# Optimization experiments

Hardware: AMD Instinct MI355X
Metric: run time of the kernel (lower is better)

The kernel has to match this reference:

```python
import jax, jax.numpy as jnp
from jax import lax
import numpy as np

B, C, H, W = 4, 128, 256, 256
HEADS = 8
MID = 256


def conv2d(x, w, stride=1, pad=0, groups=1, mode='zeros'):
    if pad:
        m = 'reflect' if mode == 'reflect' else 'constant'
        x = jnp.pad(x, ((0, 0), (0, 0), (pad, pad), (pad, pad)), mode=m)
    return lax.conv_general_dilated(
        x, w, (stride, stride), 'VALID',
        dimension_numbers=('NCHW', 'OIHW', 'NCHW'),
        feature_group_count=groups)


def layernorm(x, w, b, eps=1e-5):
    # torch LayerNorm over channel dim (applied to b (hw) c layout)
    mu = jnp.mean(x, axis=1, keepdims=True)
    var = jnp.mean((x - mu) ** 2, axis=1, keepdims=True)
    xn = (x - mu) * lax.rsqrt(var + eps)
    return xn * w[None, :, None, None] + b[None, :, None, None]


def l2norm(x, eps=1e-12):
    n = jnp.sqrt(jnp.sum(x * x, axis=-1, keepdims=True))
    return x / jnp.maximum(n, eps)


def setup_inputs() -> dict:
    key = jax.random.key(0)
    ks = jax.random.split(key, 20)
    s = 0.02
    inp = {
        'x': jax.random.normal(ks[0], (B, C, H, W), jnp.float32),
        'illu_feat': jax.random.uniform(ks[1], (B, C, H, W), jnp.float32),
        'ln1_w': jnp.ones((C,), jnp.float32),
        'ln1_b': jnp.zeros((C,), jnp.float32),
        'q_w': jax.random.normal(ks[2], (C, 1, 3, 3), jnp.float32) * s,
        'k_w': jax.random.normal(ks[3], (C, C, 3, 3), jnp.float32) * s,
        'v_w': jax.random.normal(ks[4], (C, C, 1, 1), jnp.float32) * s,
        'a1_w': jax.random.normal(ks[5], (C, 1, 3, 3), jnp.float32) * s,
        'a2_w': jax.random.normal(ks[6], (C // 2, C, 1, 1), jnp.float32) * s,
        'a2_b': jnp.zeros((C // 2,), jnp.float32),
        'temp_a': jnp.ones((HEADS, 1, 1), jnp.float32),
        'temp_v': jnp.ones((HEADS, 1, 1), jnp.float32),
        'po_w': jax.random.normal(ks[7], (C, C, 1, 1), jnp.float32) * s,
        'ln2_w': jnp.ones((C,), jnp.float32),
        'ln2_b': jnp.zeros((C,), jnp.float32),
        'p1_w': jax.random.normal(ks[8], (MID, C, 1, 1), jnp.float32) * s,
        'p1_b': jnp.zeros((MID,), jnp.float32),
        'dw_w': jax.random.normal(ks[9], (MID, 1, 3, 3), jnp.float32) * s,
        'dw_b': jnp.zeros((MID,), jnp.float32),
        'p2_w': jax.random.normal(ks[10], (C, MID, 1, 1), jnp.float32) * s,
        'p2_b': jnp.zeros((C,), jnp.float32),
    }
    return inp


def reference(x, illu_feat, ln1_w, ln1_b, q_w, k_w, v_w, a1_w, a2_w, a2_b,
              temp_a, temp_v, po_w, ln2_w, ln2_b, p1_w, p1_b, dw_w, dw_b,
              p2_w, p2_b):
    b, c, h, w = x.shape
    # ---- Attention branch ----
    xn = layernorm(x, ln1_w, ln1_b)
    q = conv2d(xn, q_w, stride=2, pad=1, groups=c, mode='reflect')  # (b,c,h/2,w/2)
    k = conv2d(xn, k_w, stride=2, pad=1, mode='reflect')            # (b,c,h/2,w/2)
    v = conv2d(xn, v_w) * illu_feat                                 # (b,c,h,w)
    a = conv2d(conv2d(xn, a1_w, stride=2, pad=1, groups=c, mode='reflect'), a2_w)
    a = a + a2_b[None, :, None, None]                               # (b,c/2,h/2,w/2)

    h2, w2 = q.shape[-2:]
    l4 = h2 * w2
    cp = c // HEADS            # channels per head (q,k,v)
    ca = (c // 2) // HEADS     # channels per head (a)
    qr = l2norm(q.reshape(b, HEADS, cp, l4))
    kr = l2norm(k.reshape(b, HEADS, cp, l4))
    ar = l2norm(a.reshape(b, HEADS, ca, l4))
    vr = v.reshape(b, HEADS, cp, h * w)

    attn_a = jax.nn.softmax(jnp.einsum('bhcl,bhdl->bhcd', qr, ar) * temp_a, axis=-1)
    attn_k = jax.nn.softmax(jnp.einsum('bhdl,bhcl->bhdc', ar, kr) * temp_v, axis=-1)
    out_v = jnp.einsum('bhdc,bhcm->bhdm', attn_k, vr)   # (b,h,ca,HW)
    out = jnp.einsum('bhcd,bhdm->bhcm', attn_a, out_v)  # (b,h,cp,HW)
    out = out.reshape(b, c, h, w)
    x = x + conv2d(out, po_w)

    # ---- FFN branch ----
    y = layernorm(x, ln2_w, ln2_b)
    y = conv2d(y, p1_w) + p1_b[None, :, None, None]
    y = conv2d(y, dw_w, pad=1, groups=MID) + dw_b[None, :, None, None]
    y = jax.nn.relu(y)
    y = conv2d(y, p2_w) + p2_b[None, :, None, None]
    return x + y
```

## Files before the change

kernel.cpp:

```cpp
#include <hip/hip_runtime.h>

#define BB 4
#define CC 128
#define HH 256
#define WW 256
#define HWSZ 65536
#define H2 128
#define W2 128
#define L4SZ 16384
#define MIDC 256
#define NHEADS 8

typedef __attribute__((ext_vector_type(8))) short short8;
typedef __attribute__((ext_vector_type(4))) short s16x4;
typedef __attribute__((ext_vector_type(4))) float f32x4;
typedef __attribute__((ext_vector_type(4))) unsigned u32x4;
typedef __attribute__((ext_vector_type(2))) unsigned u32x2;

__device__ __forceinline__ short f2bf(float v) {
  unsigned u = __builtin_bit_cast(unsigned, v);
  u += 0x7fffu + ((u >> 16) & 1u);
  return (short)(u >> 16);
}
__device__ __forceinline__ unsigned pk2(float a, float b) {
// ... 197 lines not shown
      int slot = g ^ ((p >> 1) & 3);
      short8 bfrag = ldsb[p * 4 + slot];
      const short* wbase = wt + (tap * 128 + (lane & 15)) * 128 + ci0 + g * 8;
#pragma unroll
      for (int m = 0; m < 8; m++) {
        short8 afrag = *(const short8*)(wbase + m * 16 * 128);
        acc[m] = __builtin_amdgcn_mfma_f32_16x16x32_bf16(afrag, bfrag, acc[m], 0, 0, 0);
      }
    }
  }
  int oy = by * 8 + py, ox = bx * 8 + pxx;
  int rb = g * 4;
#pragma unroll
  for (int m = 0; m < 8; m++)
#pragma unroll
    for (int r = 0; r < 4; r++)
      kg[(size_t)(bi * CC + m * 16 + rb + r) * L4SZ + oy * W2 + ox] = f2bf(acc[m][r]);
}

__global__ __launch_bounds__(256) void k_a2(const short* __restrict__ a1g,
                                            const float* __restrict__ w,
                                            const float* __restrict__ bias,
                                            short* __restrict__ ab) {
  __shared__ float t[CC][64];
  int blk = blockIdx.x;
  int bi = blk >> 8;
  int p0 = (blk & 255) * 64;
  for (int i = threadIdx.x; i < CC * 64; i += 256) {
    int ci = i >> 6, px = i & 63;
    t[ci][px] = b2f(a1g[(size_t)(bi * CC + ci) * L4SZ + p0 + px]);
  }
  __syncthreads();
  int px = threadIdx.x & 63;
  int co0 = ((__builtin_amdgcn_readfirstlane((int)threadIdx.x)) >> 6) << 4;
  float acc[16];
#pragma unroll
  for (int j = 0; j < 16; j++) acc[j] = 0.f;
  for (int ci = 0; ci < CC; ci++) {
    float in = t[ci][px];
#pragma unroll
    for (int j = 0; j < 16; j++) acc[j] += w[(co0 + j) * CC + ci] * in;
  }
#pragma unroll
  for (int j = 0; j < 16; j++)
    ab[(size_t)(bi * 64 + co0 + j) * L4SZ + p0 + px] = f2bf(acc[j] + bias[co0 + j]);
}

__global__ __launch_bounds__(256) void k_gram(const short* __restrict__ qg,
                                              const short* __restrict__ kg,
                                              const short* __restrict__ ag,
                                              float* __restrict__ partial) {
  __shared__ float red[4][1280];
  int blk = blockIdx.x;
  int bh = blk >> 3, chunk = blk & 7;
  int b = bh >> 3, h = bh & 7;
  int tid = threadIdx.x, lane = tid & 63, wv = tid >> 6;
  int cl = lane & 15, g = lane >> 4;
  const short* qb = qg + (size_t)(b * 128 + h * 16 + cl) * L4SZ;
  const short* kb = kg + (size_t)(b * 128 + h * 16 + cl) * L4SZ;
  const short* ar = ag + (size_t)(b * 64 + h * 8 + cl) * L4SZ;
  int k0 = chunk * 2048 + wv * 512 + g * 8;
  f32x4 t0 = {0,0,0,0}, t1 = {0,0,0,0}, t2 = {0,0,0,0}, t3 = {0,0,0,0}, t4 = {0,0,0,0};
#pragma unroll 4
  for (int ks = 0; ks < 16; ks++) {
    int ko = k0 + ks * 32;
    short8 fq = *(const short8*)(qb + ko);
    short8 fk = *(const short8*)(kb + ko);
    short8 fa = *(const short8*)(ar + ko);
    t0 = __builtin_amdgcn_mfma_f32_16x16x32_bf16(fq, fa, t0, 0, 0, 0);
    t1 = __builtin_amdgcn_mfma_f32_16x16x32_bf16(fa, fk, t1, 0, 0, 0);
    t2 = __builtin_amdgcn_mfma_f32_16x16x32_bf16(fq, fq, t2, 0, 0, 0);
    t3 = __builtin_amdgcn_mfma_f32_16x16x32_bf16(fk, fk, t3, 0, 0, 0);
    t4 = __builtin_amdgcn_mfma_f32_16x16x32_bf16(fa, fa, t4, 0, 0, 0);
  }
#pragma unroll
  for (int r = 0; r < 4; r++) {
    int flat = (g * 4 + r) * 16 + cl;
    red[wv][flat]        = t0[r];
    red[wv][256 + flat]  = t1[r];
    red[wv][512 + flat]  = t2[r];
    red[wv][768 + flat]  = t3[r];
    red[wv][1024 + flat] = t4[r];
  }
  __syncthreads();
  float* po = partial + (size_t)(bh * 8 + chunk) * 1280;
  for (int i = tid; i < 1280; i += 256)
    po[i] = red[0][i] + red[1][i] + red[2][i] + red[3][i];
}

__global__ __launch_bounds__(64) void k_softmax2(const float* __restrict__ partial,
                                                 const float* __restrict__ tA,
                                                 const float* __restrict__ tV,
                                                 float* __restrict__ attnA,
                                                 float* __restrict__ attnK) {
  __shared__ float S[1280];
  int bh = blockIdx.x;
  int h = bh & 7;
  for (int i = threadIdx.x; i < 1280; i += 64) {
    float s = 0.f;
    for (int c = 0; c < 8; c++) s += partial[(size_t)(bh * 8 + c) * 1280 + i];
    S[i] = s;
  }
  __syncthreads();
  float ta = tA[h], tv = tV[h];
  if (threadIdx.x < 16) {
    int c = threadIdx.x;
    float nq = fmaxf(sqrtf(S[512 + c * 17]), 1e-12f);
    float lg[8]; float m = -1e30f;
#pragma unroll
    for (int e = 0; e < 8; e++) {
      float na = fmaxf(sqrtf(S[1024 + e * 17]), 1e-12f);
      lg[e] = S[c * 16 + e] / (nq * na) * ta;
      m = fmaxf(m, lg[e]);
    }
    float sum = 0.f;
#pragma unroll
    for (int e = 0; e < 8; e++) { lg[e] = expf(lg[e] - m); sum += lg[e]; }
    float inv = 1.f / sum;
#pragma unroll
    for (int e = 0; e < 8; e++) attnA[(bh * 16 + c) * 8 + e] = lg[e] * inv;
  } else if (threadIdx.x < 24) {
    int e = threadIdx.x - 16;
    float na = fmaxf(sqrtf(S[1024 + e * 17]), 1e-12f);
    float lg[16]; float m = -1e30f;
#pragma unroll
    for (int c = 0; c < 16; c++) {
      float nk = fmaxf(sqrtf(S[768 + c * 17]), 1e-12f);
      lg[c] = S[256 + e * 16 + c] / (na * nk) * tv;
      m = fmaxf(m, lg[c]);
    }
    float sum = 0.f;
#pragma unroll
    for (int c = 0; c < 16; c++) { lg[c] = expf(lg[c] - m); sum += lg[c]; }
    float inv = 1.f / sum;
#pragma unroll
    for (int c = 0; c < 16; c++) attnK[(bh * 8 + e) * 16 + c] = lg[c] * inv;
  }
}

__global__ __launch_bounds__(256) void k_vx2(const short* __restrict__ xnt,
                                             const float* __restrict__ illu,
                                             const float* __restrict__ x,
                                             const short* __restrict__ vwb,
                                             const short* __restrict__ Mb,
                                             u32x4* __restrict__ x2n4,
                                             float* __restrict__ mu,
                                             float* __restrict__ rs) {
  __shared__ unsigned lds[4608];
  int blk = blockIdx.x;
  int bi = blk >> 10, p0 = (blk & 1023) * 64;
  int tid = threadIdx.x, lane = tid & 63, wv = tid >> 6;
  int cl = lane & 15, g = lane >> 4;
  int px = wv * 16 + cl;
  const u32x4* xsrc = (const u32x4*)(xnt + ((size_t)(bi * HWSZ + p0) << 7));
  for (int it = 0; it < 4; it++) {
    int idx = it * 256 + tid;
    int pp = idx >> 4, gg = idx & 15;
    u32x4 v = xsrc[pp * 16 + gg];
    ((u32x4*)lds)[pp * 16 + (gg ^ (pp & 7))] = v;
  }
  __syncthreads();
  f32x4 acc[8];
#pragma unroll
  for (int m = 0; m < 8; m++) acc[m] = (f32x4){0.f, 0.f, 0.f, 0.f};
#pragma unroll
  for (int kc = 0; kc < 4; kc++) {
    short8 bf = *(const short8*)((const short*)lds + px * 128 + (((kc * 4 + g) ^ (px & 7)) * 8));
#pragma unroll
    for (int m = 0; m < 8; m++) {
      short8 af = *(const short8*)(vwb + (m * 16 + cl) * 128 + kc * 32 + g * 8);
      acc[m] = __builtin_amdgcn_mfma_f32_16x16x32_bf16(af, bf, acc[m], 0, 0, 0);
    }
  }
  __syncthreads();
#pragma unroll
  for (int m = 0; m < 8; m++) {
    int cob = m * 16 + g * 4;
    float v0 = acc[m][0] * illu[(size_t)(bi * CC + cob + 0) * HWSZ + p0 + px];
    float v1 = acc[m][1] * illu[(size_t)(bi * CC + cob + 1) * HWSZ + p0 + px];
    float v2 = acc[m][2] * illu[(size_t)(bi * CC + cob + 2) * HWSZ + p0 + px];
    float v3 = acc[m][3] * illu[(size_t)(bi * CC + cob + 3) * HWSZ + p0 + px];
    int gi = 2 * m + (g >> 1);
    unsigned* dst = lds + px * 64 + ((gi ^ (px & 7)) << 2) + (g & 1) * 2;
    dst[0] = pk2(v0, v1);
    dst[1] = pk2(v2, v3);
  }
  __syncthreads();
  f32x4 acc2[8];
#pragma unroll
  for (int m = 0; m < 8; m++) acc2[m] = (f32x4){0.f, 0.f, 0.f, 0.f};
  const short* Mbb = Mb + bi * 16384;
#pragma unroll
  for (int kc = 0; kc < 4; kc++) {
    short8 bf = *(const short8*)((const short*)lds + px * 128 + (((kc * 4 + g) ^ (px & 7)) * 8));
#pragma unroll
    for (int m = 0; m < 8; m++) {
      short8 af = *(const short8*)(Mbb + (m * 16 + cl) * 128 + kc * 32 + g * 8);
      acc2[m] = __builtin_amdgcn_mfma_f32_16x16x32_bf16(af, bf, acc2[m], 0, 0, 0);
    }
  }
  float s = 0.f, s2 = 0.f;
  unsigned xp[16];
#pragma unroll
  for (int m = 0; m < 8; m++) {
    float tv[4];
#pragma unroll
    for (int r = 0; r < 4; r++) {
      int co = m * 16 + g * 4 + r;
      size_t gi = (size_t)(bi * CC + co) * HWSZ + p0 + px;
      float t = x[gi] + acc2[m][r];
      tv[r] = t; s += t; s2 += t * t;
    }
    xp[2 * m]     = pk2(tv[0], tv[1]);
    xp[2 * m + 1] = pk2(tv[2], tv[3]);
  }
  s  += __shfl_xor(s, 16);  s  += __shfl_xor(s, 32);
  s2 += __shfl_xor(s2, 16); s2 += __shfl_xor(s2, 32);
  float muv = s * (1.f / 128.f);
  float rsv = rsqrtf(s2 * (1.f / 128.f) - muv * muv + 1e-5f);
  if (g == 0) { mu[bi * HWSZ + p0 + px] = muv; rs[bi * HWSZ + p0 + px] = rsv; }
  __syncthreads();
#pragma unroll
  for (int m = 0; m < 8; m++) {
    lds[px * 68 + m * 8 + g * 2 + 0] = xp[2 * m];
    lds[px * 68 + m * 8 + g * 2 + 1] = xp[2 * m + 1];
  }
  __syncthreads();
  u32x4* dst4 = x2n4 + (size_t)(bi * HWSZ + p0) * 16;
  for (int it = 0; it < 4; it++) {
    int flat = it * 256 + tid;
    int pp = flat >> 4, j = flat & 15;
    dst4[flat] = *(const u32x4*)(lds + pp * 68 + j * 4);
  }
}

__global__ __launch_bounds__(256) void k_p1(const u32x4* __restrict__ x2n4,
                                            const short* __restrict__ w1p,
                                            const float* __restrict__ s1,
                                            const float* __restrict__ s2f,
                                            const float* __restrict__ mu,
                                            const float* __restrict__ rs,
                                            u32x4* __restrict__ y1n4) {
  __shared__ u32x4 bt[1024];
  __shared__ u32x4 olds[2048];
  int blk = blockIdx.x;
  int bi = blk >> 10, p0 = (blk & 1023) * 64;
  int tid = threadIdx.x, lane = tid & 63, wv = tid >> 6;
  int cl = lane & 15, g = lane >> 4;
  for (int f = tid; f < 1024; f += 256) {
    int px = f >> 4, kg = f & 15;
    bt[kg * 64 + (px ^ kg)] = x2n4[(size_t)(bi * HWSZ + p0 + px) * 16 + kg];
  }
  __syncthreads();
  f32x4 acc[4][4];
#pragma unroll
  for (int mt = 0; mt < 4; mt++)
#pragma unroll
    for (int n = 0; n < 4; n++) acc[mt][n] = (f32x4){0.f, 0.f, 0.f, 0.f};
#pragma unroll
  for (int kc = 0; kc < 4; kc++) {
    short8 bfr[4];
#pragma unroll
    for (int n = 0; n < 4; n++) {
      int px = n * 16 + cl, kgi = kc * 4 + g;
      bfr[n] = __builtin_bit_cast(short8, bt[kgi * 64 + (px ^ kgi)]);
    }
#pragma unroll
    for (int mt = 0; mt < 4; mt++) {
      short8 af = *(const short8*)(w1p + (wv * 64 + mt * 16 + cl) * 128 + kc * 32 + g * 8);
#pragma unroll
      for (int n = 0; n < 4; n++)
        acc[mt][n] = __builtin_amdgcn_mfma_f32_16x16x32_bf16(af, bfr[n], acc[mt][n], 0, 0, 0);
    }
  }
  float muv[4], rsv[4];
#pragma unroll
  for (int n = 0; n < 4; n++) {
    muv[n] = mu[bi * HWSZ + p0 + n * 16 + cl];
    rsv[n] = rs[bi * HWSZ + p0 + n * 16 + cl];
  }
#pragma unroll
  for (int mt = 0; mt < 4; mt++) {
    int mid = wv * 64 + mt * 16 + g * 4;
    float4 s1v = *(const float4*)(s1 + mid);
    float4 s2v = *(const float4*)(s2f + mid);
    int gi = wv * 8 + mt * 2 + (g >> 1);
#pragma unroll
    for (int n = 0; n < 4; n++) {
      int px = n * 16 + cl;
      float y0 = rsv[n] * (acc[mt][n][0] - muv[n] * s1v.x) + s2v.x;
      float y1 = rsv[n] * (acc[mt][n][1] - muv[n] * s1v.y) + s2v.y;
      float y2 = rsv[n] * (acc[mt][n][2] - muv[n] * s1v.z) + s2v.z;
      float y3 = rsv[n] * (acc[mt][n][3] - muv[n] * s1v.w) + s2v.w;
      unsigned* dp = (unsigned*)&olds[px * 32 + (gi ^ (px & 7))] + (g & 1) * 2;
      dp[0] = pk2(y0, y1);
      dp[1] = pk2(y2, y3);
    }
  }
  __syncthreads();
  u32x4* dst = y1n4 + (size_t)(bi * HWSZ + p0) * 32;
  for (int it = 0; it < 8; it++) {
    int f = it * 256 + tid;
    int px = f >> 5, gi = f & 31;
    dst[f] = olds[px * 32 + (gi ^ (px & 7))];
  }
}

__global__ __launch_bounds__(256) void k_ffn2(const u32x4* __restrict__ y1n4,
                                              const float* __restrict__ dwwt,
                                              const float* __restrict__ dwb,
                                              const short* __restrict__ p2wb,
                                              const float* __restrict__ p2b,
                                              const u32x4* __restrict__ x2n4,
                                              float* __restrict__ out) {
  __shared__ u32x4 ylds[1600];
  __shared__ u32x4 dwt[1024];
  int blk = blockIdx.x;
  int tx = blk & 31, ty = (blk >> 5) & 31, b = blk >> 10;
  int r0 = ty * 8 - 1, c0 = tx * 8 - 1;
  int tid = threadIdx.x, lane = tid & 63, wv = tid >> 6;
  int cl = lane & 15, g = lane >> 4;
  int pp = tid & 63;
  int qy = pp >> 3, qx = pp & 7;
  f32x4 acc[2][4];
#pragma unroll
  for (int mt = 0; mt < 2; mt++)
#pragma unroll
    for (int n = 0; n < 4; n++) acc[mt][n] = (f32x4){0.f, 0.f, 0.f, 0.f};
  for (int ch = 0; ch < 2; ch++) {
    if (ch) __syncthreads();
    for (int i = tid; i < 1600; i += 256) {
      int p = i >> 4, gg = i & 15;
      int rr = p / 10, cc = p - rr * 10;
      int gr = r0 + rr, gc = c0 + cc;
      u32x4 v = (u32x4){0u, 0u, 0u, 0u};
      if (gr >= 0 && gr < HH && gc >= 0 && gc < WW)
        v = y1n4[(size_t)(b * HWSZ + gr * WW + gc) * 32 + ch * 16 + gg];
      ylds[p * 16 + (gg ^ (p & 7))] = v;
    }
    __syncthreads();
    float sdw[32];
#pragma unroll
    for (int j = 0; j < 32; j++) sdw[j] = 0.f;
#pragma unroll
    for (int tap = 0; tap < 9; tap++) {
      int dy = tap / 3, dx = tap - 3 * dy;
      int p = (qy + dy) * 10 + qx + dx;
      const float* wp = dwwt + tap * 256 + ch * 128 + wv * 32;
#pragma unroll
      for (int q = 0; q < 4; q++) {
        u32x4 vv = ylds[p * 16 + ((wv * 4 + q) ^ (p & 7))];
        sdw[q * 8 + 0] += wp[q * 8 + 0] * bflo(vv.x);
        sdw[q * 8 + 1] += wp[q * 8 + 1] * bfhi(vv.x);
        sdw[q * 8 + 2] += wp[q * 8 + 2] * bflo(vv.y);
        sdw[q * 8 + 3] += wp[q * 8 + 3] * bfhi(vv.y);
        sdw[q * 8 + 4] += wp[q * 8 + 4] * bflo(vv.z);
        sdw[q * 8 + 5] += wp[q * 8 + 5] * bfhi(vv.z);
        sdw[q * 8 + 6] += wp[q * 8 + 6] * bflo(vv.w);
        sdw[q * 8 + 7] += wp[q * 8 + 7] * bfhi(vv.w);
      }
    }
    const float* db = dwb + ch * 128 + wv * 32;
#pragma unroll
    for (int q = 0; q < 4; q++) {
      u32x4 pkv;
      pkv.x = pk2(fmaxf(sdw[q * 8 + 0] + db[q * 8 + 0], 0.f), fmaxf(sdw[q * 8 + 1] + db[q * 8 + 1], 0.f));
      pkv.y = pk2(fmaxf(sdw[q * 8 + 2] + db[q * 8 + 2], 0.f), fmaxf(sdw[q * 8 + 3] + db[q * 8 + 3], 0.f));
      pkv.z = pk2(fmaxf(sdw[q * 8 + 4] + db[q * 8 + 4], 0.f), fmaxf(sdw[q * 8 + 5] + db[q * 8 + 5], 0.f));
      pkv.w = pk2(fmaxf(sdw[q * 8 + 6] + db[q * 8 + 6], 0.f), fmaxf(sdw[q * 8 + 7] + db[q * 8 + 7], 0.f));
      dwt[pp * 16 + ((wv * 4 + q) ^ (pp & 7))] = pkv;
    }
    __syncthreads();
#pragma unroll
    for (int kc = 0; kc < 4; kc++) {
      short8 af0 = *(const short8*)(p2wb + (wv * 32 + cl) * 256 + ch * 128 + kc * 32 + g * 8);
      short8 af1 = *(const short8*)(p2wb + (wv * 32 + 16 + cl) * 256 + ch * 128 + kc * 32 + g * 8);
#pragma unroll
      for (int n = 0; n < 4; n++) {
        int px = n * 16 + cl;
        short8 bf = __builtin_bit_cast(short8, dwt[px * 16 + ((kc * 4 + g) ^ (px & 7))]);
        acc[0][n] = __builtin_amdgcn_mfma_f32_16x16x32_bf16(af0, bf, acc[0][n], 0, 0, 0);
        acc[1][n] = __builtin_amdgcn_mfma_f32_16x16x32_bf16(af1, bf, acc[1][n], 0, 0, 0);
      }
    }
  }
#pragma unroll
  for (int mt = 0; mt < 2; mt++) {
    int cob = wv * 32 + mt * 16 + g * 4;
    float pb0 = p2b[cob + 0], pb1 = p2b[cob + 1], pb2 = p2b[cob + 2], pb3 = p2b[cob + 3];
#pragma unroll
    for (int n = 0; n < 4; n++) {
      int px = n * 16 + cl;
      int oy = ty * 8 + (px >> 3), ox = tx * 8 + (px & 7);
      size_t gp = (size_t)b * HWSZ + oy * WW + ox;
      const unsigned* xr = (const unsigned*)(x2n4 + gp * 16 + (cob >> 3));
      unsigned xa = xr[(g & 1) * 2 + 0], xb2 = xr[(g & 1) * 2 + 1];
      size_t gi = (size_t)(b * CC + cob) * HWSZ + oy * WW + ox;
      out[gi]             = bflo(xa)  + acc[mt][n][0] + pb0;
      out[gi + HWSZ]      = bfhi(xa)  + acc[mt][n][1] + pb1;
      out[gi + 2 * HWSZ]  = bflo(xb2) + acc[mt][n][2] + pb2;
      out[gi + 3 * HWSZ]  = bfhi(xb2) + acc[mt][n][3] + pb3;
    }
  }
}

extern "C" void kernel_launch(void* const* d_in, const int* in_sizes, int n_in,
                              void* d_out, int out_size, void* d_ws, size_t ws_size,
                              hipStream_t stream) {
  const float* x    = (const float*)d_in[0];
  const float* illu = (const float*)d_in[1];
  const float* ln1w = (const float*)d_in[2];
  const float* ln1b = (const float*)d_in[3];
  const float* qw   = (const float*)d_in[4];
  const float* kw   = (const float*)d_in[5];
  const float* vw   = (const float*)d_in[6];
  const float* a1w  = (const float*)d_in[7];
  const float* a2w  = (const float*)d_in[8];
  const float* a2b  = (const float*)d_in[9];
  const float* tA   = (const float*)d_in[10];
  const float* tV   = (const float*)d_in[11];
  const float* pow_ = (const float*)d_in[12];
  const float* ln2w = (const float*)d_in[13];
  const float* ln2b = (const float*)d_in[14];
  const float* p1w  = (const float*)d_in[15];
  const float* p1b  = (const float*)d_in[16];
  const float* dww  = (const float*)d_in[17];
  const float* dwb  = (const float*)d_in[18];
  const float* p2w  = (const float*)d_in[19];
  const float* p2b  = (const float*)d_in[20];
  float* out = (float*)d_out;

  float* ws    = (float*)d_ws;
  u32x4* x2n4  = (u32x4*)ws;
  float* mu    = ws + 16777216;
  float* rs    = ws + 17039360;
  float* attnA = ws + 17301504;
  float* attnK = ws + 17305600;
  short* vwb   = (short*)(ws + 17309696);
  short* w1p   = (short*)(ws + 17317888);
  short* p2wb  = (short*)(ws + 17334272);
  short* Mb    = (short*)(ws + 17350656);
  float* s1    = ws + 17383424;
  float* s2f   = ws + 17383680;
  short* wt    = (short*)(ws + 17383936);
  float* qwt   = ws + 17457664;
  float* a1wt  = ws + 17458816;
  float* dwwt  = ws + 17459968;
  u32x4* y1n4  = (u32x4*)(ws + 17462272);
  short* xnt   = (short*)(ws + 17462272);
  short* qg    = (short*)(ws + 34239488);
  short* kgb   = (short*)(ws + 38433792);
  short* a1g   = (short*)(ws + 42628096);
  short* ab    = (short*)(ws + 46822400);
  float* partial = ws + 48919552;

  k_ln1<<<4096, 256, 0, stream>>>(x, ln1w, ln1b, xnt);
  k_wcast<<<576, 256, 0, stream>>>(kw, wt);
  k_prep1<<<340, 256, 0, stream>>>(vw, p1w, ln2w, ln2b, p1b, p2w, qw, a1w, dww,
                                   vwb, w1p, p2wb, s1, s2f, qwt, a1wt, dwwt);
  k_dwsn<<<1024, 256, 0, stream>>>(xnt, qwt, a1wt, qg, a1g);
  k_kconv_mfma<<<1024, 256, 0, stream>>>(xnt, wt, kgb);
  k_a2<<<1024, 256, 0, stream>>>(a1g, a2w, a2b, ab);
  k_gram<<<256, 256, 0, stream>>>(qg, kgb, ab, partial);
  k_softmax2<<<32, 64, 0, stream>>>(partial, tA, tV, attnA, attnK);
  k_prep2<<<4, 256, 0, stream>>>(pow_, attnA, attnK, Mb);
  k_vx2<<<4096, 256, 0, stream>>>(xnt, illu, x, vwb, Mb, x2n4, mu, rs);
  k_p1<<<4096, 256, 0, stream>>>(x2n4, w1p, s1, s2f, mu, rs, y1n4);
  k_ffn2<<<4096, 256, 0, stream>>>(y1n4, dwwt, dwb, p2wb, p2b, x2n4, out);
}
```

Baseline: 739.4 us.

## Prefetch illu/x loads in k_vx2 and halve k_ffn2 LDS chunking

In k_vx2, the illu and residual x values are loaded into registers before the matmuls, so their global-memory latency overlaps the MFMA work instead of sitting in the epilogue. In k_ffn2, the 256 mid channels are processed in four chunks of 64 instead of two of 128. This halves the shared-memory buffers and the depthwise accumulator registers, and uses new XOR swizzles to avoid LDS bank conflicts. The aim is higher occupancy, at the cost of more halo reloads and more barriers.

```diff
diff --git a/kernel.cpp b/kernel.cpp
--- a/kernel.cpp
+++ b/kernel.cpp
@@ -373,6 +373,12 @@
   int tid = threadIdx.x, lane = tid & 63, wv = tid >> 6;
   int cl = lane & 15, g = lane >> 4;
   int px = wv * 16 + cl;
+  float ilv[32];
+#pragma unroll
+  for (int m = 0; m < 8; m++)
+#pragma unroll
+    for (int r = 0; r < 4; r++)
+      ilv[m * 4 + r] = illu[(size_t)(bi * CC + m * 16 + g * 4 + r) * HWSZ + p0 + px];
   const u32x4* xsrc = (const u32x4*)(xnt + ((size_t)(bi * HWSZ + p0) << 7));
   for (int it = 0; it < 4; it++) {
     int idx = it * 256 + tid;
@@ -396,17 +402,22 @@
   __syncthreads();
 #pragma unroll
   for (int m = 0; m < 8; m++) {
-    int cob = m * 16 + g * 4;
-    float v0 = acc[m][0] * illu[(size_t)(bi * CC + cob + 0) * HWSZ + p0 + px];
-    float v1 = acc[m][1] * illu[(size_t)(bi * CC + cob + 1) * HWSZ + p0 + px];
-    float v2 = acc[m][2] * illu[(size_t)(bi * CC + cob + 2) * HWSZ + p0 + px];
-    float v3 = acc[m][3] * illu[(size_t)(bi * CC + cob + 3) * HWSZ + p0 + px];
+    float v0 = acc[m][0] * ilv[m * 4 + 0];
+    float v1 = acc[m][1] * ilv[m * 4 + 1];
+    float v2 = acc[m][2] * ilv[m * 4 + 2];
+    float v3 = acc[m][3] * ilv[m * 4 + 3];
     int gi = 2 * m + (g >> 1);
     unsigned* dst = lds + px * 64 + ((gi ^ (px & 7)) << 2) + (g & 1) * 2;
     dst[0] = pk2(v0, v1);
     dst[1] = pk2(v2, v3);
   }
   __syncthreads();
+  float xv[32];
+#pragma unroll
+  for (int m = 0; m < 8; m++)
+#pragma unroll
+    for (int r = 0; r < 4; r++)
+      xv[m * 4 + r] = x[(size_t)(bi * CC + m * 16 + g * 4 + r) * HWSZ + p0 + px];
   f32x4 acc2[8];
 #pragma unroll
   for (int m = 0; m < 8; m++) acc2[m] = (f32x4){0.f, 0.f, 0.f, 0.f};
@@ -427,9 +438,7 @@
     float tv[4];
 #pragma unroll
     for (int r = 0; r < 4; r++) {
-      int co = m * 16 + g * 4 + r;
-      size_t gi = (size_t)(bi * CC + co) * HWSZ + p0 + px;
-      float t = x[gi] + acc2[m][r];
+      float t = xv[m * 4 + r] + acc2[m][r];
       tv[r] = t; s += t; s2 += t * t;
     }
     xp[2 * m]     = pk2(tv[0], tv[1]);
@@ -534,8 +543,8 @@
                                               const float* __restrict__ p2b,
                                               const u32x4* __restrict__ x2n4,
                                               float* __restrict__ out) {
-  __shared__ u32x4 ylds[1600];
-  __shared__ u32x4 dwt[1024];
+  __shared__ u32x4 ylds[800];
+  __shared__ u32x4 dwt[512];
   int blk = blockIdx.x;
   int tx = blk & 31, ty = (blk >> 5) & 31, b = blk >> 10;
   int r0 = ty * 8 - 1, c0 = tx * 8 - 1;
@@ -543,67 +552,67 @@
   int cl = lane & 15, g = lane >> 4;
   int pp = tid & 63;
   int qy = pp >> 3, qx = pp & 7;
+  int ppsw = (pp ^ (pp >> 3)) & 7;
   f32x4 acc[2][4];
 #pragma unroll
   for (int mt = 0; mt < 2; mt++)
 #pragma unroll
     for (int n = 0; n < 4; n++) acc[mt][n] = (f32x4){0.f, 0.f, 0.f, 0.f};
-  for (int ch = 0; ch < 2; ch++) {
-    if (ch) __syncthreads();
-    for (int i = tid; i < 1600; i += 256) {
-      int p = i >> 4, gg = i & 15;
+  for (int ch = 0; ch < 4; ch++) {
+    for (int i = tid; i < 800; i += 256) {
+      int p = i >> 3, gg = i & 7;
       int rr = p / 10, cc = p - rr * 10;
       int gr = r0 + rr, gc = c0 + cc;
       u32x4 v = (u32x4){0u, 0u, 0u, 0u};
       if (gr >= 0 && gr < HH && gc >= 0 && gc < WW)
-        v = y1n4[(size_t)(b * HWSZ + gr * WW + gc) * 32 + ch * 16 + gg];
-      ylds[p * 16 + (gg ^ (p & 7))] = v;
+        v = y1n4[(size_t)(b * HWSZ + gr * WW + gc) * 32 + ch * 8 + gg];
+      ylds[p * 8 + (gg ^ ((p * 3) & 7))] = v;
     }
     __syncthreads();
-    float sdw[32];
-#pragma unroll
-    for (int j = 0; j < 32; j++) sdw[j] = 0.f;
-#pragma unroll
-    for (int tap = 0; tap < 9; tap++) {
-      int dy = tap / 3, dx = tap - 3 * dy;
-      int p = (qy + dy) * 10 + qx + dx;
-      const float* wp = dwwt + tap * 256 + ch * 128 + wv * 32;
-#pragma unroll
-      for (int q = 0; q < 4; q++) {
-        u32x4 vv = ylds[p * 16 + ((wv * 4 + q) ^ (p & 7))];
-        sdw[q * 8 + 0] += wp[q * 8 + 0] * bflo(vv.x);
-        sdw[q * 8 + 1] += wp[q * 8 + 1] * bfhi(vv.x);
-        sdw[q * 8 + 2] += wp[q * 8 + 2] * bflo(vv.y);
-        sdw[q * 8 + 3] += wp[q * 8 + 3] * bfhi(vv.y);
-        sdw[q * 8 + 4] += wp[q * 8 + 4] * bflo(vv.z);
-        sdw[q * 8 + 5] += wp[q * 8 + 5] * bfhi(vv.z);
-        sdw[q * 8 + 6] += wp[q * 8 + 6] * bflo(vv.w);
-        sdw[q * 8 + 7] += wp[q * 8 + 7] * bfhi(vv.w);
+#pragma unroll
+    for (int e = 0; e < 2; e++) {
+      int gran = wv * 2 + e;
+      float sdw[8];
+#pragma unroll
+      for (int j = 0; j < 8; j++) sdw[j] = 0.f;
+#pragma unroll
+      for (int tap = 0; tap < 9; tap++) {
+        int dy = tap / 3, dx = tap - 3 * dy;
+        int p = (qy + dy) * 10 + qx + dx;
+        u32x4 vv = ylds[p * 8 + (gran ^ ((p * 3) & 7))];
+        const float* wp = dwwt + tap * 256 + ch * 64 + gran * 8;
+        sdw[0] += wp[0] * bflo(vv.x);
+        sdw[1] += wp[1] * bfhi(vv.x);
+        sdw[2] += wp[2] * bflo(vv.y);
+        sdw[3] += wp[3] * bfhi(vv.y);
+        sdw[4] += wp[4] * bflo(vv.z);
+        sdw[5] += wp[5] * bfhi(vv.z);
+        sdw[6] += wp[6] * bflo(vv.w);
+        sdw[7] += wp[7] * bfhi(vv.w);
       }
-    }
-    const float* db = dwb + ch * 128 + wv * 32;
-#pragma unroll
-    for (int q = 0; q < 4; q++) {
+      const float* db = dwb + ch * 64 + gran * 8;
       u32x4 pkv;
-      pkv.x = pk2(fmaxf(sdw[q * 8 + 0] + db[q * 8 + 0], 0.f), fmaxf(sdw[q * 8 + 1] + db[q * 8 + 1], 0.f));
-      pkv.y = pk2(fmaxf(sdw[q * 8 + 2] + db[q * 8 + 2], 0.f), fmaxf(sdw[q * 8 + 3] + db[q * 8 + 3], 0.f));
-      pkv.z = pk2(fmaxf(sdw[q * 8 + 4] + db[q * 8 + 4], 0.f), fmaxf(sdw[q * 8 + 5] + db[q * 8 + 5], 0.f));
-      pkv.w = pk2(fmaxf(sdw[q * 8 + 6] + db[q * 8 + 6], 0.f), fmaxf(sdw[q * 8 + 7] + db[q * 8 + 7], 0.f));
-      dwt[pp * 16 + ((wv * 4 + q) ^ (pp & 7))] = pkv;
+      pkv.x = pk2(fmaxf(sdw[0] + db[0], 0.f), fmaxf(sdw[1] + db[1], 0.f));
+      pkv.y = pk2(fmaxf(sdw[2] + db[2], 0.f), fmaxf(sdw[3] + db[3], 0.f));
+      pkv.z = pk2(fmaxf(sdw[4] + db[4], 0.f), fmaxf(sdw[5] + db[5], 0.f));
+      pkv.w = pk2(fmaxf(sdw[6] + db[6], 0.f), fmaxf(sdw[7] + db[7], 0.f));
+      dwt[pp * 8 + (gran ^ ppsw)] = pkv;
     }
     __syncthreads();
 #pragma unroll
-    for (int kc = 0; kc < 4; kc++) {
-      short8 af0 = *(const short8*)(p2wb + (wv * 32 + cl) * 256 + ch * 128 + kc * 32 + g * 8);
-      short8 af1 = *(const short8*)(p2wb + (wv * 32 + 16 + cl) * 256 + ch * 128 + kc * 32 + g * 8);
+    for (int kc = 0; kc < 2; kc++) {
+      short8 af0 = *(const short8*)(p2wb + (wv * 32 + cl) * 256 + ch * 64 + kc * 32 + g * 8);
+      short8 af1 = *(const short8*)(p2wb + (wv * 32 + 16 + cl) * 256 + ch * 64 + kc * 32 + g * 8);
+      int gi = kc * 4 + g;
 #pragma unroll
       for (int n = 0; n < 4; n++) {
         int px = n * 16 + cl;
-        short8 bf = __builtin_bit_cast(short8, dwt[px * 16 + ((kc * 4 + g) ^ (px & 7))]);
+        short8 bf = __builtin_bit_cast(short8, dwt[px * 8 + (gi ^ ((px ^ (px >> 3)) & 7))]);
         acc[0][n] = __builtin_amdgcn_mfma_f32_16x16x32_bf16(af0, bf, acc[0][n], 0, 0, 0);
         acc[1][n] = __builtin_amdgcn_mfma_f32_16x16x32_bf16(af1, bf, acc[1][n], 0, 0, 0);
       }
     }
+    __syncthreads();
   }
 #pragma unroll
   for (int mt = 0; mt < 2; mt++) {
```

New measurement: 761.9 us. 3.1% more time.

## Split fused depthwise+pointwise FFN kernel into separate dw and p2 kernels

Applied to the files above, without the earlier changes.

Replaces the fused depthwise-3x3 plus pointwise-conv kernel with two kernels: a direct-from-global depthwise conv writing a bf16 intermediate, and an MFMA pointwise GEMM over linear 64-pixel tiles. This removes the halo tile staging and the per-half synchronization in the fused kernel. In exchange it adds a full write and read of a 256-channel bf16 intermediate to global memory, plus one more launch.

```diff
diff --git a/kernel.cpp b/kernel.cpp
--- a/kernel.cpp
+++ b/kernel.cpp
@@ -527,82 +527,91 @@
   }
 }
 
-__global__ __launch_bounds__(256) void k_ffn2(const u32x4* __restrict__ y1n4,
-                                              const float* __restrict__ dwwt,
-                                              const float* __restrict__ dwb,
-                                              const short* __restrict__ p2wb,
-                                              const float* __restrict__ p2b,
-                                              const u32x4* __restrict__ x2n4,
-                                              float* __restrict__ out) {
-  __shared__ u32x4 ylds[1600];
-  __shared__ u32x4 dwt[1024];
-  int blk = blockIdx.x;
-  int tx = blk & 31, ty = (blk >> 5) & 31, b = blk >> 10;
-  int r0 = ty * 8 - 1, c0 = tx * 8 - 1;
+__global__ __launch_bounds__(256) void k_dw(const u32x4* __restrict__ y1n4,
+                                            const float* __restrict__ dwwt,
+                                            const float* __restrict__ dwb,
+                                            u32x4* __restrict__ y2n4) {
+  int blk = blockIdx.x;
+  int bi = blk >> 10, p0 = (blk & 1023) * 64;
+  int tid = threadIdx.x;
+  int px = tid >> 2, q4 = tid & 3;
+  int p = p0 + px;
+  int gy = p >> 8, gx = p & 255;
+  float acc[64];
+#pragma unroll
+  for (int j = 0; j < 64; j++) acc[j] = 0.f;
+#pragma unroll
+  for (int dy = 0; dy < 3; dy++) {
+    int ry = gy + dy - 1;
+    if (ry < 0 || ry >= HH) continue;
+#pragma unroll
+    for (int dx = 0; dx < 3; dx++) {
+      int rx = gx + dx - 1;
+      if (rx < 0 || rx >= WW) continue;
+      const u32x4* src = y1n4 + (size_t)(bi * HWSZ + ry * WW + rx) * 32 + q4 * 8;
+      const float4* wp4 = (const float4*)(dwwt + (dy * 3 + dx) * 256 + q4 * 64);
+#pragma unroll
+      for (int e = 0; e < 8; e++) {
+        u32x4 v = src[e];
+        float4 w0 = wp4[e * 2], w1 = wp4[e * 2 + 1];
+        acc[e * 8 + 0] += w0.x * bflo(v.x);
+        acc[e * 8 + 1] += w0.y * bfhi(v.x);
+        acc[e * 8 + 2] += w0.z * bflo(v.y);
+        acc[e * 8 + 3] += w0.w * bfhi(v.y);
+        acc[e * 8 + 4] += w1.x * bflo(v.z);
+        acc[e * 8 + 5] += w1.y * bfhi(v.z);
+        acc[e * 8 + 6] += w1.z * bflo(v.w);
+        acc[e * 8 + 7] += w1.w * bfhi(v.w);
+      }
+    }
+  }
+  const float* db = dwb + q4 * 64;
+  u32x4* dst = y2n4 + (size_t)(bi * HWSZ + p) * 32 + q4 * 8;
+#pragma unroll
+  for (int e = 0; e < 8; e++) {
+    u32x4 pkv;
+    pkv.x = pk2(fmaxf(acc[e * 8 + 0] + db[e * 8 + 0], 0.f), fmaxf(acc[e * 8 + 1] + db[e * 8 + 1], 0.f));
+    pkv.y = pk2(fmaxf(acc[e * 8 + 2] + db[e * 8 + 2], 0.f), fmaxf(acc[e * 8 + 3] + db[e * 8 + 3], 0.f));
+    pkv.z = pk2(fmaxf(acc[e * 8 + 4] + db[e * 8 + 4], 0.f), fmaxf(acc[e * 8 + 5] + db[e * 8 + 5], 0.f));
+    pkv.w = pk2(fmaxf(acc[e * 8 + 6] + db[e * 8 + 6], 0.f), fmaxf(acc[e * 8 + 7] + db[e * 8 + 7], 0.f));
+    dst[e] = pkv;
+  }
+}
+
+__global__ __launch_bounds__(256) void k_p2(const u32x4* __restrict__ y2n4,
+                                            const short* __restrict__ p2wb,
+                                            const float* __restrict__ p2b,
+                                            const u32x4* __restrict__ x2n4,
+                                            float* __restrict__ out) {
+  __shared__ u32x4 bt[2048];
+  int blk = blockIdx.x;
+  int bi = blk >> 10, p0 = (blk & 1023) * 64;
   int tid = threadIdx.x, lane = tid & 63, wv = tid >> 6;
   int cl = lane & 15, g = lane >> 4;
-  int pp = tid & 63;
-  int qy = pp >> 3, qx = pp & 7;
+  for (int f = tid; f < 2048; f += 256) {
+    int px = f >> 5, kg = f & 31;
+    bt[kg * 64 + (px ^ (kg & 15))] = y2n4[(size_t)(bi * HWSZ + p0 + px) * 32 + kg];
+  }
+  __syncthreads();
   f32x4 acc[2][4];
 #pragma unroll
   for (int mt = 0; mt < 2; mt++)
 #pragma unroll
     for (int n = 0; n < 4; n++) acc[mt][n] = (f32x4){0.f, 0.f, 0.f, 0.f};
-  for (int ch = 0; ch < 2; ch++) {
-    if (ch) __syncthreads();
-    for (int i = tid; i < 1600; i += 256) {
-      int p = i >> 4, gg = i & 15;
-      int rr = p / 10, cc = p - rr * 10;
-      int gr = r0 + rr, gc = c0 + cc;
-      u32x4 v = (u32x4){0u, 0u, 0u, 0u};
-      if (gr >= 0 && gr < HH && gc >= 0 && gc < WW)
-        v = y1n4[(size_t)(b * HWSZ + gr * WW + gc) * 32 + ch * 16 + gg];
-      ylds[p * 16 + (gg ^ (p & 7))] = v;
-    }
-    __syncthreads();
-    float sdw[32];
-#pragma unroll
-    for (int j = 0; j < 32; j++) sdw[j] = 0.f;
-#pragma unroll
-    for (int tap = 0; tap < 9; tap++) {
-      int dy = tap / 3, dx = tap - 3 * dy;
-      int p = (qy + dy) * 10 + qx + dx;
-      const float* wp = dwwt + tap * 256 + ch * 128 + wv * 32;
-#pragma unroll
-      for (int q = 0; q < 4; q++) {
-        u32x4 vv = ylds[p * 16 + ((wv * 4 + q) ^ (p & 7))];
-        sdw[q * 8 + 0] += wp[q * 8 + 0] * bflo(vv.x);
-        sdw[q * 8 + 1] += wp[q * 8 + 1] * bfhi(vv.x);
-        sdw[q * 8 + 2] += wp[q * 8 + 2] * bflo(vv.y);
-        sdw[q * 8 + 3] += wp[q * 8 + 3] * bfhi(vv.y);
-        sdw[q * 8 + 4] += wp[q * 8 + 4] * bflo(vv.z);
-        sdw[q * 8 + 5] += wp[q * 8 + 5] * bfhi(vv.z);
-        sdw[q * 8 + 6] += wp[q * 8 + 6] * bflo(vv.w);
-        sdw[q * 8 + 7] += wp[q * 8 + 7] * bfhi(vv.w);
-      }
-    }
-    const float* db = dwb + ch * 128 + wv * 32;
-#pragma unroll
-    for (int q = 0; q < 4; q++) {
-      u32x4 pkv;
-      pkv.x = pk2(fmaxf(sdw[q * 8 + 0] + db[q * 8 + 0], 0.f), fmaxf(sdw[q * 8 + 1] + db[q * 8 + 1], 0.f));
-      pkv.y = pk2(fmaxf(sdw[q * 8 + 2] + db[q * 8 + 2], 0.f), fmaxf(sdw[q * 8 + 3] + db[q * 8 + 3], 0.f));
-      pkv.z = pk2(fmaxf(sdw[q * 8 + 4] + db[q * 8 + 4], 0.f), fmaxf(sdw[q * 8 + 5] + db[q * 8 + 5], 0.f));
-      pkv.w = pk2(fmaxf(sdw[q * 8 + 6] + db[q * 8 + 6], 0.f), fmaxf(sdw[q * 8 + 7] + db[q * 8 + 7], 0.f));
-      dwt[pp * 16 + ((wv * 4 + q) ^ (pp & 7))] = pkv;
-    }
-    __syncthreads();
-#pragma unroll
-    for (int kc = 0; kc < 4; kc++) {
-      short8 af0 = *(const short8*)(p2wb + (wv * 32 + cl) * 256 + ch * 128 + kc * 32 + g * 8);
-      short8 af1 = *(const short8*)(p2wb + (wv * 32 + 16 + cl) * 256 + ch * 128 + kc * 32 + g * 8);
-#pragma unroll
-      for (int n = 0; n < 4; n++) {
-        int px = n * 16 + cl;
-        short8 bf = __builtin_bit_cast(short8, dwt[px * 16 + ((kc * 4 + g) ^ (px & 7))]);
-        acc[0][n] = __builtin_amdgcn_mfma_f32_16x16x32_bf16(af0, bf, acc[0][n], 0, 0, 0);
-        acc[1][n] = __builtin_amdgcn_mfma_f32_16x16x32_bf16(af1, bf, acc[1][n], 0, 0, 0);
-      }
+#pragma unroll
+  for (int kc = 0; kc < 8; kc++) {
+    short8 bfr[4];
+#pragma unroll
+    for (int n = 0; n < 4; n++) {
+      int pxn = n * 16 + cl, kgi = kc * 4 + g;
+      bfr[n] = __builtin_bit_cast(short8, bt[kgi * 64 + (pxn ^ (kgi & 15))]);
+    }
+#pragma unroll
+    for (int mt = 0; mt < 2; mt++) {
+      short8 af = *(const short8*)(p2wb + (wv * 32 + mt * 16 + cl) * 256 + kc * 32 + g * 8);
+#pragma unroll
+      for (int n = 0; n < 4; n++)
+        acc[mt][n] = __builtin_amdgcn_mfma_f32_16x16x32_bf16(af, bfr[n], acc[mt][n], 0, 0, 0);
     }
   }
 #pragma unroll
@@ -611,12 +620,11 @@
     float pb0 = p2b[cob + 0], pb1 = p2b[cob + 1], pb2 = p2b[cob + 2], pb3 = p2b[cob + 3];
 #pragma unroll
     for (int n = 0; n < 4; n++) {
-      int px = n * 16 + cl;
-      int oy = ty * 8 + (px >> 3), ox = tx * 8 + (px & 7);
-      size_t gp = (size_t)b * HWSZ + oy * WW + ox;
+      int pxn = n * 16 + cl;
+      size_t gp = (size_t)bi * HWSZ + p0 + pxn;
       const unsigned* xr = (const unsigned*)(x2n4 + gp * 16 + (cob >> 3));
       unsigned xa = xr[(g & 1) * 2 + 0], xb2 = xr[(g & 1) * 2 + 1];
-      size_t gi = (size_t)(b * CC + cob) * HWSZ + oy * WW + ox;
+      size_t gi = (size_t)(bi * CC + cob) * HWSZ + p0 + pxn;
       out[gi]             = bflo(xa)  + acc[mt][n][0] + pb0;
       out[gi + HWSZ]      = bfhi(xa)  + acc[mt][n][1] + pb1;
       out[gi + 2 * HWSZ]  = bflo(xb2) + acc[mt][n][2] + pb2;
@@ -674,6 +682,7 @@
   short* a1g   = (short*)(ws + 42628096);
   short* ab    = (short*)(ws + 46822400);
   float* partial = ws + 48919552;
+  u32x4* y2n4  = (u32x4*)(ws + 51016704);
 
   k_ln1<<<4096, 256, 0, stream>>>(x, ln1w, ln1b, xnt);
   k_wcast<<<576, 256, 0, stream>>>(kw, wt);
@@ -687,5 +696,6 @@
   k_prep2<<<4, 256, 0, stream>>>(pow_, attnA, attnK, Mb);
   k_vx2<<<4096, 256, 0, stream>>>(xnt, illu, x, vwb, Mb, x2n4, mu, rs);
   k_p1<<<4096, 256, 0, stream>>>(x2n4, w1p, s1, s2f, mu, rs, y1n4);
-  k_ffn2<<<4096, 256, 0, stream>>>(y1n4, dwwt, dwb, p2wb, p2b, x2n4, out);
-}
+  k_dw<<<4096, 256, 0, stream>>>(y1n4, dwwt, dwb, y2n4);
+  k_p2<<<4096, 256, 0, stream>>>(y2n4, p2wb, p2b, x2n4, out);
+}
```

Result: slower. 1.064 ms (+44.0%).

## Prefetch second channel half into registers and swizzle block order in ffn2

Applied to the files above, without the earlier changes.

Unrolls the two-channel-half loop in k_ffn2 and issues the global loads for the second half's halo tile into registers before the first half's depthwise conv finishes. Those registers are written to shared memory while the MFMA pass over the first half runs, hiding global latency. Block indices are also remapped so consecutive blocks land on different image regions or batches, which changes L2 and XCD locality. The prefetch adds 7 u32x4 registers per thread, which raises VGPR pressure and may lower occupancy.

```diff
diff --git a/kernel.cpp b/kernel.cpp
--- a/kernel.cpp
+++ b/kernel.cpp
@@ -536,7 +536,8 @@
                                               float* __restrict__ out) {
   __shared__ u32x4 ylds[1600];
   __shared__ u32x4 dwt[1024];
-  int blk = blockIdx.x;
+  int j = blockIdx.x;
+  int blk = ((j & 7) << 9) + (j >> 3);
   int tx = blk & 31, ty = (blk >> 5) & 31, b = blk >> 10;
   int r0 = ty * 8 - 1, c0 = tx * 8 - 1;
   int tid = threadIdx.x, lane = tid & 63, wv = tid >> 6;
@@ -548,40 +549,55 @@
   for (int mt = 0; mt < 2; mt++)
 #pragma unroll
     for (int n = 0; n < 4; n++) acc[mt][n] = (f32x4){0.f, 0.f, 0.f, 0.f};
-  for (int ch = 0; ch < 2; ch++) {
-    if (ch) __syncthreads();
-    for (int i = tid; i < 1600; i += 256) {
+
+  for (int i = tid; i < 1600; i += 256) {
+    int p = i >> 4, gg = i & 15;
+    int rr = p / 10, cc = p - rr * 10;
+    int gr = r0 + rr, gc = c0 + cc;
+    u32x4 v = (u32x4){0u, 0u, 0u, 0u};
+    if (gr >= 0 && gr < HH && gc >= 0 && gc < WW)
+      v = y1n4[(size_t)(b * HWSZ + gr * WW + gc) * 32 + gg];
+    ylds[p * 16 + (gg ^ (p & 7))] = v;
+  }
+  __syncthreads();
+
+  float sdw[32];
+#pragma unroll
+  for (int jj = 0; jj < 32; jj++) sdw[jj] = 0.f;
+#pragma unroll
+  for (int tap = 0; tap < 9; tap++) {
+    int dy = tap / 3, dx = tap - 3 * dy;
+    int p = (qy + dy) * 10 + qx + dx;
+    const float* wp = dwwt + tap * 256 + wv * 32;
+#pragma unroll
+    for (int q = 0; q < 4; q++) {
+      u32x4 vv = ylds[p * 16 + ((wv * 4 + q) ^ (p & 7))];
+      sdw[q * 8 + 0] += wp[q * 8 + 0] * bflo(vv.x);
+      sdw[q * 8 + 1] += wp[q * 8 + 1] * bfhi(vv.x);
+      sdw[q * 8 + 2] += wp[q * 8 + 2] * bflo(vv.y);
+      sdw[q * 8 + 3] += wp[q * 8 + 3] * bfhi(vv.y);
+      sdw[q * 8 + 4] += wp[q * 8 + 4] * bflo(vv.z);
+      sdw[q * 8 + 5] += wp[q * 8 + 5] * bfhi(vv.z);
+      sdw[q * 8 + 6] += wp[q * 8 + 6] * bflo(vv.w);
+      sdw[q * 8 + 7] += wp[q * 8 + 7] * bfhi(vv.w);
+    }
+  }
+  u32x4 pf[7];
+#pragma unroll
+  for (int it = 0; it < 7; it++) {
+    int i = it * 256 + tid;
+    u32x4 v = (u32x4){0u, 0u, 0u, 0u};
+    if (i < 1600) {
       int p = i >> 4, gg = i & 15;
       int rr = p / 10, cc = p - rr * 10;
       int gr = r0 + rr, gc = c0 + cc;
-      u32x4 v = (u32x4){0u, 0u, 0u, 0u};
       if (gr >= 0 && gr < HH && gc >= 0 && gc < WW)
-        v = y1n4[(size_t)(b * HWSZ + gr * WW + gc) * 32 + ch * 16 + gg];
-      ylds[p * 16 + (gg ^ (p & 7))] = v;
-    }
-    __syncthreads();
-    float sdw[32];
-#pragma unroll
-    for (int j = 0; j < 32; j++) sdw[j] = 0.f;
-#pragma unroll
-    for (int tap = 0; tap < 9; tap++) {
-      int dy = tap / 3, dx = tap - 3 * dy;
-      int p = (qy + dy) * 10 + qx + dx;
-      const float* wp = dwwt + tap * 256 + ch * 128 + wv * 32;
-#pragma unroll
-      for (int q = 0; q < 4; q++) {
-        u32x4 vv = ylds[p * 16 + ((wv * 4 + q) ^ (p & 7))];
-        sdw[q * 8 + 0] += wp[q * 8 + 0] * bflo(vv.x);
-        sdw[q * 8 + 1] += wp[q * 8 + 1] * bfhi(vv.x);
-        sdw[q * 8 + 2] += wp[q * 8 + 2] * bflo(vv.y);
-        sdw[q * 8 + 3] += wp[q * 8 + 3] * bfhi(vv.y);
-        sdw[q * 8 + 4] += wp[q * 8 + 4] * bflo(vv.z);
-        sdw[q * 8 + 5] += wp[q * 8 + 5] * bfhi(vv.z);
-        sdw[q * 8 + 6] += wp[q * 8 + 6] * bflo(vv.w);
-        sdw[q * 8 + 7] += wp[q * 8 + 7] * bfhi(vv.w);
-      }
-    }
-    const float* db = dwb + ch * 128 + wv * 32;
+        v = y1n4[(size_t)(b * HWSZ + gr * WW + gc) * 32 + 16 + gg];
+    }
+    pf[it] = v;
+  }
+  {
+    const float* db = dwb + wv * 32;
 #pragma unroll
     for (int q = 0; q < 4; q++) {
       u32x4 pkv;
@@ -591,18 +607,72 @@
       pkv.w = pk2(fmaxf(sdw[q * 8 + 6] + db[q * 8 + 6], 0.f), fmaxf(sdw[q * 8 + 7] + db[q * 8 + 7], 0.f));
       dwt[pp * 16 + ((wv * 4 + q) ^ (pp & 7))] = pkv;
     }
-    __syncthreads();
-#pragma unroll
-    for (int kc = 0; kc < 4; kc++) {
-      short8 af0 = *(const short8*)(p2wb + (wv * 32 + cl) * 256 + ch * 128 + kc * 32 + g * 8);
-      short8 af1 = *(const short8*)(p2wb + (wv * 32 + 16 + cl) * 256 + ch * 128 + kc * 32 + g * 8);
-#pragma unroll
-      for (int n = 0; n < 4; n++) {
-        int px = n * 16 + cl;
-        short8 bf = __builtin_bit_cast(short8, dwt[px * 16 + ((kc * 4 + g) ^ (px & 7))]);
-        acc[0][n] = __builtin_amdgcn_mfma_f32_16x16x32_bf16(af0, bf, acc[0][n], 0, 0, 0);
-        acc[1][n] = __builtin_amdgcn_mfma_f32_16x16x32_bf16(af1, bf, acc[1][n], 0, 0, 0);
-      }
+  }
+  __syncthreads();
+#pragma unroll
+  for (int it = 0; it < 7; it++) {
+    int i = it * 256 + tid;
+    if (i < 1600) {
+      int p = i >> 4, gg = i & 15;
+      ylds[p * 16 + (gg ^ (p & 7))] = pf[it];
+    }
+  }
+#pragma unroll
+  for (int kc = 0; kc < 4; kc++) {
+    short8 af0 = *(const short8*)(p2wb + (wv * 32 + cl) * 256 + kc * 32 + g * 8);
+    short8 af1 = *(const short8*)(p2wb + (wv * 32 + 16 + cl) * 256 + kc * 32 + g * 8);
+#pragma unroll
+    for (int n = 0; n < 4; n++) {
+      int px = n * 16 + cl;
+      short8 bf = __builtin_bit_cast(short8, dwt[px * 16 + ((kc * 4 + g) ^ (px & 7))]);
+      acc[0][n] = __builtin_amdgcn_mfma_f32_16x16x32_bf16(af0, bf, acc[0][n], 0, 0, 0);
+      acc[1][n] = __builtin_amdgcn_mfma_f32_16x16x32_bf16(af1, bf, acc[1][n], 0, 0, 0);
+    }
+  }
+  __syncthreads();
+#pragma unroll
+  for (int jj = 0; jj < 32; jj++) sdw[jj] = 0.f;
+#pragma unroll
+  for (int tap = 0; tap < 9; tap++) {
+    int dy = tap / 3, dx = tap - 3 * dy;
+    int p = (qy + dy) * 10 + qx + dx;
+    const float* wp = dwwt + tap * 256 + 128 + wv * 32;
+#pragma unroll
+    for (int q = 0; q < 4; q++) {
+      u32x4 vv = ylds[p * 16 + ((wv * 4 + q) ^ (p & 7))];
+      sdw[q * 8 + 0] += wp[q * 8 + 0] * bflo(vv.x);
+      sdw[q * 8 + 1] += wp[q * 8 + 1] * bfhi(vv.x);
+      sdw[q * 8 + 2] += wp[q * 8 + 2] * bflo(vv.y);
+      sdw[q * 8 + 3] += wp[q * 8 + 3] * bfhi(vv.y);
+      sdw[q * 8 + 4] += wp[q * 8 + 4] * bflo(vv.z);
+      sdw[q * 8 + 5] += wp[q * 8 + 5] * bfhi(vv.z);
+      sdw[q * 8 + 6] += wp[q * 8 + 6] * bflo(vv.w);
+      sdw[q * 8 + 7] += wp[q * 8 + 7] * bfhi(vv.w);
+    }
+  }
+  {
+    const float* db = dwb + 128 + wv * 32;
+#pragma unroll
+    for (int q = 0; q < 4; q++) {
+      u32x4 pkv;
+      pkv.x = pk2(fmaxf(sdw[q * 8 + 0] + db[q * 8 + 0], 0.f), fmaxf(sdw[q * 8 + 1] + db[q * 8 + 1], 0.f));
+      pkv.y = pk2(fmaxf(sdw[q * 8 + 2] + db[q * 8 + 2], 0.f), fmaxf(sdw[q * 8 + 3] + db[q * 8 + 3], 0.f));
+      pkv.z = pk2(fmaxf(sdw[q * 8 + 4] + db[q * 8 + 4], 0.f), fmaxf(sdw[q * 8 + 5] + db[q * 8 + 5], 0.f));
+      pkv.w = pk2(fmaxf(sdw[q * 8 + 6] + db[q * 8 + 6], 0.f), fmaxf(sdw[q * 8 + 7] + db[q * 8 + 7], 0.f));
+      dwt[pp * 16 + ((wv * 4 + q) ^ (pp & 7))] = pkv;
+    }
+  }
+  __syncthreads();
+#pragma unroll
+  for (int kc = 0; kc < 4; kc++) {
+    short8 af0 = *(const short8*)(p2wb + (wv * 32 + cl) * 256 + 128 + kc * 32 + g * 8);
+    short8 af1 = *(const short8*)(p2wb + (wv * 32 + 16 + cl) * 256 + 128 + kc * 32 + g * 8);
+#pragma unroll
+    for (int n = 0; n < 4; n++) {
+      int px = n * 16 + cl;
+      short8 bf = __builtin_bit_cast(short8, dwt[px * 16 + ((kc * 4 + g) ^ (px & 7))]);
+      acc[0][n] = __builtin_amdgcn_mfma_f32_16x16x32_bf16(af0, bf, acc[0][n], 0, 0, 0);
+      acc[1][n] = __builtin_amdgcn_mfma_f32_16x16x32_bf16(af1, bf, acc[1][n], 0, 0, 0);
     }
   }
 #pragma unroll
```

Result: slower. 791.5 us (+7.0%).
